# Optimization experiments

Measured on AMD Instinct MI355X. Metric: run time of the kernel, lower is better.

Reference implementation:

```python
import jax, jax.numpy as jnp
import numpy as np

BS, N, N_HEAD, F_IN, F_OUT = 8, 1024, 8, 256, 64
NEG_SLOPE = 0.2


def setup_inputs() -> dict:
    key = jax.random.key(0)
    k_h, k_adj, k_w, k_src, k_dst = jax.random.split(key, 5)
    h = jax.random.normal(k_h, (BS, N, F_IN), dtype=jnp.float32)
    adj = jax.random.randint(k_adj, (BS, N, N), 0, 2) > 0  # bool adjacency
    # xavier_uniform-style params
    def xavier(k, shape, fan_in, fan_out):
        limit = float(np.sqrt(6.0 / (fan_in + fan_out)))
        return jax.random.uniform(k, shape, jnp.float32, -limit, limit)
    w = xavier(k_w, (N_HEAD, F_IN, F_OUT), F_IN, F_OUT)
    a_src = xavier(k_src, (N_HEAD, F_OUT, 1), F_OUT, 1)
    a_dst = xavier(k_dst, (N_HEAD, F_OUT, 1), F_OUT, 1)
    bias = jnp.zeros((F_OUT,), dtype=jnp.float32)
    return {"h": h, "adj": adj, "w": w, "a_src": a_src, "a_dst": a_dst, "bias": bias}


def reference(h, adj, w, a_src, a_dst, bias):
    # h: [bs, n, f_in], w: [n_head, f_in, f_out]
    h_prime = jnp.einsum('bnf,hfo->bhno', h, w)            # [bs, h, n, f_out]
    t = jnp.tanh(h_prime)
    attn_src = jnp.einsum('bhno,ho->bhn', t, a_src[..., 0])  # [bs, h, n]
    attn_dst = jnp.einsum('bhno,ho->bhn', t, a_dst[..., 0])  # [bs, h, n]
    attn = attn_src[:, :, :, None] + attn_dst[:, :, None, :]  # [bs, h, n, n]
    attn = jnp.where(attn >= 0, attn, NEG_SLOPE * attn)       # leaky_relu(0.2)
    n = adj.shape[-1]
    mask = ~(adj[:, None, :, :] | jnp.eye(n, dtype=bool))     # [bs, 1->h, n, n]
    attn = jnp.where(mask, -jnp.inf, attn)
    attn = jax.nn.softmax(attn, axis=-1)                      # diag always valid
    out = jnp.einsum('bhnm,bhmo->bhno', attn, h_prime)
    return out + bias
```

## Files before the change

### kernel.cpp

```cpp
#include <hip/hip_runtime.h>
#include <math.h>

#define BS 8
#define NPTS 1024
#define NH 8
#define FIN 256
#define FOUT 64

typedef __attribute__((ext_vector_type(8))) short s8v;
typedef __attribute__((ext_vector_type(8))) _Float16 h8v;
typedef __attribute__((ext_vector_type(2))) __fp16 fp16x2;
typedef __attribute__((ext_vector_type(4))) float f4v;
typedef unsigned long long u64;

__device__ __forceinline__ unsigned short f2bf(float f) {
  unsigned u = __float_as_uint(f);
  return (unsigned short)((u + 0x7fffu + ((u >> 16) & 1u)) >> 16);
}
__device__ __forceinline__ float bf2f(unsigned short s) {
  return __uint_as_float(((unsigned)s) << 16);
}
__device__ __forceinline__ float fast_tanh(float x) {
  float e = __expf(2.f * x);
  return 1.f - 2.f / (e + 1.f);
}
__device__ __forceinline__ float hw_exp2(float x) {
  float r;
  asm("v_exp_f32 %0, %1" : "=v"(r) : "v"(x));
  return r;
}

__device__ __forceinline__ void gl_lds16(const void* g, void* l) {
  __builtin_amdgcn_global_load_lds(
      (const __attribute__((address_space(1))) unsigned*)g,
      (__attribute__((address_space(3))) unsigned*)l, 16, 0, 0);
}

__global__ __launch_bounds__(256) void prep_kernel(
    const void* __restrict__ adjv, const float* __restrict__ w,
    const float* __restrict__ h,
    u64* __restrict__ abits,
    unsigned short* __restrict__ wT_hi, unsigned short* __restrict__ wT_lo,
    unsigned short* __restrict__ hs_hi, unsigned short* __restrict__ hs_lo)
{
  const int blk = blockIdx.x;
  const int t = threadIdx.x;
  if (blk < 2048) {
    __shared__ int badsh;
    if (t == 0) badsh = 0;
    __syncthreads();
    if (((const unsigned*)adjv)[t] > 1u) badsh = 1;
    __syncthreads();
    const int lane = t & 63;
    const int gw = blk * 4 + (t >> 6);
    const int b = gw >> 10, i = gw & 1023;
    const int m16 = lane & 15, g = lane >> 4;
    u64 words[4];
    if (badsh == 0) {
      const int4* row4 = (const int4*)((const int*)adjv + ((size_t)b * NPTS + i) * NPTS);
      int4 av[4];
      av[0] = row4[lane]; av[1] = row4[lane + 64];
      av[2] = row4[lane + 128]; av[3] = row4[lane + 192];
#pragma unroll
      for (int ci = 0; ci < 4; ++ci) {
        unsigned n = (unsigned)(av[ci].x != 0) | ((unsigned)(av[ci].y != 0) << 1) |
                     ((unsigned)(av[ci].z != 0) << 2) | ((unsigned)(av[ci].w != 0) << 3);
        unsigned d = (unsigned)(i - (ci * 256 + 4 * lane));
        if (d < 4u) n |= 1u << d;
        u64 val = (u64)n << (4 * m16);
#pragma unroll
        for (int msk = 1; msk <= 8; msk <<= 1)
          val |= (u64)__shfl_xor(val, msk, 64);
        words[ci] = val;
      }
    } else {
      const unsigned* rowB = (const unsigned*)((const unsigned char*)adjv + ((size_t)b * NPTS + i) * NPTS);
      unsigned av[4];
      av[0] = rowB[lane]; av[1] = rowB[lane + 64];
      av[2] = rowB[lane + 128]; av[3] = rowB[lane + 192];
#pragma unroll
      for (int ci = 0; ci < 4; ++ci) {
        unsigned v = av[ci];
        unsigned n = ((v & 0xffu) ? 1u : 0u) | (((v >> 8) & 0xffu) ? 2u : 0u) |
                     (((v >> 16) & 0xffu) ? 4u : 0u) | ((v >> 24) ? 8u : 0u);
        unsigned d = (unsigned)(i - (ci * 256 + 4 * lane));
        if (d < 4u) n |= 1u << d;
        u64 val = (u64)n << (4 * m16);
#pragma unroll
        for (int msk = 1; msk <= 8; msk <<= 1)
          val |= (u64)__shfl_xor(val, msk, 64);
        words[ci] = val;
      }
    }
    if (m16 == 0) {
#pragma unroll
      for (int ci = 0; ci < 4; ++ci)
        abits[((size_t)b * NPTS + i) * 16 + ci * 4 + g] = words[ci];
    }
  } else if (blk < 2112) {
    const int bb = blk - 2048;
    const int hh = bb >> 3, ks = bb & 7;
    const int o = t & 63, kq = t >> 6;
#pragma unroll
    for (int e = 0; e < 8; ++e) {
      int k = ks * 32 + kq * 8 + e;
      float v = w[((size_t)hh * FIN + k) * FOUT + o];
      unsigned short hi = f2bf(v);
      wT_hi[((size_t)hh * FOUT + o) * FIN + k] = hi;
      wT_lo[((size_t)hh * FOUT + o) * FIN + k] = f2bf(v - bf2f(hi));
    }
  } else {
    const size_t g = (size_t)(blk - 2112) * 256 + t;
    const float4* hp4 = (const float4*)h + g * 2;
    float4 v0 = hp4[0], v1 = hp4[1];
    float vv[8] = {v0.x, v0.y, v0.z, v0.w, v1.x, v1.y, v1.z, v1.w};
    unsigned short hb[8], lb[8];
#pragma unroll
    for (int e = 0; e < 8; ++e) {
      unsigned u = __float_as_uint(vv[e]);
      float r = vv[e] - __uint_as_float(u & 0xffff0000u);
      hb[e] = (unsigned short)(u >> 16);
      lb[e] = (unsigned short)(__float_as_uint(r) >> 16);
    }
    *(uint4*)(hs_hi + g * 8) = *(const uint4*)&hb[0];
    *(uint4*)(hs_lo + g * 8) = *(const uint4*)&lb[0];
  }
}

__global__ __launch_bounds__(256, 4) void proj_kernel(
    const unsigned short* __restrict__ hs_hi, const unsigned short* __restrict__ hs_lo,
    const unsigned short* __restrict__ wT_hi, const unsigned short* __restrict__ wT_lo,
    const float* __restrict__ a_src, const float* __restrict__ a_dst,
    unsigned short* __restrict__ hfrag,
    float* __restrict__ srcb, float* __restrict__ dstb)
{
  __shared__ unsigned short Bbuf[2][4096];
  __shared__ float tile[64][65];

  const int t = threadIdx.x;
  const int lane = t & 63;
  const int wv = t >> 6;
  const int blk = blockIdx.x;
  const int it = blk & 15;
  const int hh = (blk >> 4) & 7;
  const int b  = blk >> 7;
  const int i0 = it * 64;
  const int bh = b * NH + hh;
  const int l15 = lane & 15;
  const int g4  = lane >> 4;
  const int koff = g4 * 8;

  const int o_t  = t >> 2;
  const int gsrc = (t & 3) ^ ((o_t >> 1) & 3);
  const unsigned short* gB_hi = wT_hi + ((size_t)(hh * FOUT + o_t)) * FIN + gsrc * 8;
  const unsigned short* gB_lo = wT_lo + ((size_t)(hh * FOUT + o_t)) * FIN + gsrc * 8;

  const unsigned short* arow_hi = hs_hi + ((size_t)(b * NPTS + i0 + wv * 16 + l15)) * FIN + koff;
  const unsigned short* arow_lo = hs_lo + ((size_t)(b * NPTS + i0 + wv * 16 + l15)) * FIN + koff;

  const int sw = (l15 >> 1) & 3;
  int roff[4];
#pragma unroll
  for (int nt = 0; nt < 4; ++nt)
    roff[nt] = (nt * 16 + l15) * 32 + (g4 ^ sw) * 8;

  gl_lds16(gB_hi, &Bbuf[0][wv * 512]);
  gl_lds16(gB_lo, &Bbuf[0][2048 + wv * 512]);
  s8v Ah = *(const s8v*)(arow_hi);
  s8v Al = *(const s8v*)(arow_lo);

  f4v acc[4];
#pragma unroll
  for (int nt = 0; nt < 4; ++nt) acc[nt] = 0.0f;
  __syncthreads();

#pragma unroll
  for (int k0 = 0; k0 < 8; ++k0) {
    const int buf = k0 & 1;
    s8v Ah_n = Ah, Al_n = Al;
    if (k0 < 7) {
      gl_lds16(gB_hi + (k0 + 1) * 32, &Bbuf[buf ^ 1][wv * 512]);
      gl_lds16(gB_lo + (k0 + 1) * 32, &Bbuf[buf ^ 1][2048 + wv * 512]);
      Ah_n = *(const s8v*)(arow_hi + (k0 + 1) * 32);
      Al_n = *(const s8v*)(arow_lo + (k0 + 1) * 32);
    }
    const unsigned short* fb = &Bbuf[buf][0];
#pragma unroll
    for (int nt = 0; nt < 4; ++nt) {
      s8v Bh = *(const s8v*)(fb + roff[nt]);
      s8v Bl = *(const s8v*)(fb + 2048 + roff[nt]);
      acc[nt] = __builtin_amdgcn_mfma_f32_16x16x32_bf16(Ah, Bh, acc[nt], 0, 0, 0);
      acc[nt] = __builtin_amdgcn_mfma_f32_16x16x32_bf16(Al, Bh, acc[nt], 0, 0, 0);
      acc[nt] = __builtin_amdgcn_mfma_f32_16x16x32_bf16(Ah, Bl, acc[nt], 0, 0, 0);
    }
    Ah = Ah_n; Al = Al_n;
    __syncthreads();
  }

  float a_s[4], a_d[4];
#pragma unroll
  for (int nt = 0; nt < 4; ++nt) {
    a_s[nt] = a_src[hh * FOUT + nt * 16 + l15];
    a_d[nt] = a_dst[hh * FOUT + nt * 16 + l15];
  }
#pragma unroll
  for (int qq = 0; qq < 4; ++qq) {
    float ps = 0.f, pd = 0.f;
#pragma unroll
    for (int nt = 0; nt < 4; ++nt) {
      float tv = fast_tanh(acc[nt][qq]);
      ps = fmaf(tv, a_s[nt], ps);
      pd = fmaf(tv, a_d[nt], pd);
    }
#pragma unroll
    for (int m = 8; m >= 1; m >>= 1) {
      ps += __shfl_xor(ps, m, 64);
      pd += __shfl_xor(pd, m, 64);
    }
    if (l15 == 0) {
      int row = i0 + wv * 16 + g4 * 4 + qq;
      srcb[(size_t)bh * NPTS + row] = ps;
      dstb[(size_t)bh * NPTS + row] = pd;
    }
  }

#pragma unroll
  for (int nt = 0; nt < 4; ++nt)
#pragma unroll
    for (int qq = 0; qq < 4; ++qq)
      tile[wv * 16 + g4 * 4 + qq][nt * 16 + l15] = acc[nt][qq];
  __syncthreads();

  const int cbase = t >> 6;
#pragma unroll
  for (int ci = 0; ci < 2; ++ci) {
    int cc = cbase + ci * 4;
    int ks = cc >> 2, nt2 = cc & 3;
    int jb = ks * 32 + ((lane >> 4) * 8);
    int ob = nt2 * 16 + l15;
    h8v v;
#pragma unroll
    for (int e = 0; e < 8; ++e) v[e] = (_Float16)tile[jb + e][ob];
    *(h8v*)(hfrag + (((size_t)(bh * 16 + it) * 8 + cc) * 64 + lane) * 8) = v;
  }
}

__global__ __launch_bounds__(256, 4) void attn_kernel(
    const u64* __restrict__ abits,
    const unsigned short* __restrict__ hfrag,
    const float* __restrict__ srcb, const float* __restrict__ dstb,
    const float* __restrict__ bias, float* __restrict__ out)
{
  __shared__ float dsh[NPTS];
  __shared__ float wred[4];
  __shared__ uint2 mlut[16];
  __shared__ unsigned short frag[2][4096];

  const int t = threadIdx.x;
  const int lane = t & 63;
  const int wv = t >> 6;
  const int blk = blockIdx.x;
  const int it = blk & 15;
  const int hh = (blk >> 4) & 7;
  const int b  = blk >> 7;
  const int i0 = it * 64;
  const int bh = b * NH + hh;
  const int l15 = lane & 15;
  const int koff = (lane >> 4) * 8;
  const int rowA = i0 + wv * 16 + l15;

  const uint4* fgb = (const uint4*)hfrag + (size_t)bh * 16 * 512;
  const u64* abrow = abits + ((size_t)b * NPTS + rowA) * 16;

  uint4 s0 = fgb[t];
  uint4 s1 = fgb[t + 256];
  u64 ab_cur = abrow[0];
  const float src_r = srcb[(size_t)bh * NPTS + rowA];
  float4 dv = ((const float4*)(dstb + (size_t)bh * NPTS))[t];

  if (t < 16) {
    unsigned m = t;
    mlut[t] = make_uint2(
        ((m & 1u) ? 0xFFFFu : 0u) | (((m >> 1) & 1u) ? 0xFFFF0000u : 0u),
        (((m >> 2) & 1u) ? 0xFFFFu : 0u) | (((m >> 3) & 1u) ? 0xFFFF0000u : 0u));
  }

  const float L2E = 1.44269504f;
  float4 dsc;
  dsc.x = dv.x * L2E; dsc.y = dv.y * L2E; dsc.z = dv.z * L2E; dsc.w = dv.w * L2E;
  ((float4*)dsh)[t] = dsc;
  float lm = fmaxf(fmaxf(dv.x, dv.y), fmaxf(dv.z, dv.w));
#pragma unroll
  for (int m = 32; m >= 1; m >>= 1) lm = fmaxf(lm, __shfl_xor(lm, m, 64));
  if (lane == 0) wred[wv] = lm;
  __syncthreads();
  const float M = fmaxf(fmaxf(wred[0], wred[1]), fmaxf(wred[2], wred[3]));
  const float xm = src_r + M;
  const float m_row = fmaxf(xm, 0.2f * xm);
  const float c1s = (src_r - m_row) * L2E;
  const float c2s = (0.2f * src_r - m_row) * L2E;

  ((uint4*)&frag[0][0])[t]       = s0;
  ((uint4*)&frag[0][0])[t + 256] = s1;
  __syncthreads();

  h8v ones;
#pragma unroll
  for (int e = 0; e < 8; ++e) ones[e] = (_Float16)1.0f;

  f4v acc[4], acc_l;
#pragma unroll
  for (int nt = 0; nt < 4; ++nt) acc[nt] = 0.0f;
  acc_l = 0.0f;

#pragma unroll 2
  for (int jt = 0; jt < 16; ++jt) {
    const int buf = jt & 1;
    uint4 n0, n1; u64 ab_nxt;
    if (jt < 15) {
      const uint4* fgn = fgb + (size_t)(jt + 1) * 512;
      n0 = fgn[t];
      n1 = fgn[t + 256];
      ab_nxt = abrow[jt + 1];
    }
    __builtin_amdgcn_sched_barrier(0);

    const int jb = jt * 64 + koff;
    float4 d0 = *(const float4*)&dsh[jb];
    float4 d1 = *(const float4*)&dsh[jb + 4];
    float4 d2 = *(const float4*)&dsh[jb + 32];
    float4 d3 = *(const float4*)&dsh[jb + 36];
    float dl0[8] = {d0.x, d0.y, d0.z, d0.w, d1.x, d1.y, d1.z, d1.w};
    float dl1[8] = {d2.x, d2.y, d2.z, d2.w, d3.x, d3.y, d3.z, d3.w};
    const unsigned w0 = (unsigned)(ab_cur) >> koff;
    const unsigned w1 = (unsigned)(ab_cur >> 32) >> koff;
    float pe0[8], pe1[8];
#pragma unroll
    for (int e = 0; e < 8; ++e) {
      float arg = fmaxf(c1s + dl0[e], fmaf(0.2f, dl0[e], c2s));
      pe0[e] = hw_exp2(arg);
    }
#pragma unroll
    for (int e = 0; e < 8; ++e) {
      float arg = fmaxf(c1s + dl1[e], fmaf(0.2f, dl1[e], c2s));
      pe1[e] = hw_exp2(arg);
    }
    union { fp16x2 q[4]; unsigned u[4]; h8v v; } ua, ub;
    ua.q[0] = __builtin_amdgcn_cvt_pkrtz(pe0[0], pe0[1]);
    ua.q[1] = __builtin_amdgcn_cvt_pkrtz(pe0[2], pe0[3]);
    ua.q[2] = __builtin_amdgcn_cvt_pkrtz(pe0[4], pe0[5]);
    ua.q[3] = __builtin_amdgcn_cvt_pkrtz(pe0[6], pe0[7]);
    ub.q[0] = __builtin_amdgcn_cvt_pkrtz(pe1[0], pe1[1]);
    ub.q[1] = __builtin_amdgcn_cvt_pkrtz(pe1[2], pe1[3]);
    ub.q[2] = __builtin_amdgcn_cvt_pkrtz(pe1[4], pe1[5]);
    ub.q[3] = __builtin_amdgcn_cvt_pkrtz(pe1[6], pe1[7]);
    {
      uint2 ma0 = mlut[w0 & 15], ma1 = mlut[(w0 >> 4) & 15];
      uint2 mb0 = mlut[w1 & 15], mb1 = mlut[(w1 >> 4) & 15];
      ua.u[0] &= ma0.x; ua.u[1] &= ma0.y; ua.u[2] &= ma1.x; ua.u[3] &= ma1.y;
      ub.u[0] &= mb0.x; ub.u[1] &= mb0.y; ub.u[2] &= mb1.x; ub.u[3] &= mb1.y;
    }
    h8v pa0 = ua.v;
    h8v pa1 = ub.v;

    __builtin_amdgcn_s_setprio(1);
#pragma unroll
    for (int nt = 0; nt < 4; ++nt) {
      h8v B0 = *(const h8v*)&frag[buf][(nt * 64 + lane) * 8];
      acc[nt] = __builtin_amdgcn_mfma_f32_16x16x32_f16(pa0, B0, acc[nt], 0, 0, 0);
    }
    acc_l = __builtin_amdgcn_mfma_f32_16x16x32_f16(pa0, ones, acc_l, 0, 0, 0);
#pragma unroll
    for (int nt = 0; nt < 4; ++nt) {
      h8v B1 = *(const h8v*)&frag[buf][((4 + nt) * 64 + lane) * 8];
      acc[nt] = __builtin_amdgcn_mfma_f32_16x16x32_f16(pa1, B1, acc[nt], 0, 0, 0);
    }
    acc_l = __builtin_amdgcn_mfma_f32_16x16x32_f16(pa1, ones, acc_l, 0, 0, 0);
    __builtin_amdgcn_s_setprio(0);

    if (jt < 15) {
      ((uint4*)&frag[buf ^ 1][0])[t]       = n0;
      ((uint4*)&frag[buf ^ 1][0])[t + 256] = n1;
      ab_cur = ab_nxt;
    }
    __syncthreads();
  }

  float bias4[4];
#pragma unroll
  for (int nt = 0; nt < 4; ++nt) bias4[nt] = bias[nt * 16 + l15];

#pragma unroll
  for (int qq = 0; qq < 4; ++qq) {
    float linv = 1.0f / acc_l[qq];
    int rowq = i0 + wv * 16 + (lane >> 4) * 4 + qq;
    size_t ob = ((size_t)bh * NPTS + rowq) * FOUT;
#pragma unroll
    for (int nt = 0; nt < 4; ++nt)
      out[ob + nt * 16 + l15] = acc[nt][qq] * linv + bias4[nt];
  }
}

extern "C" void kernel_launch(void* const* d_in, const int* in_sizes, int n_in,
                              void* d_out, int out_size, void* d_ws, size_t ws_size,
                              hipStream_t stream)
{
  const float* h     = (const float*)d_in[0];
  const void*  adj   = d_in[1];
  const float* w     = (const float*)d_in[2];
  const float* a_src = (const float*)d_in[3];
  const float* a_dst = (const float*)d_in[4];
  const float* bias  = (const float*)d_in[5];
  float* out = (float*)d_out;

  char* p = (char*)d_ws;
  float* srcb = (float*)p;                      p += (size_t)BS * NH * NPTS * 4;
  float* dstb = (float*)p;                      p += (size_t)BS * NH * NPTS * 4;
  unsigned short* wT_hi = (unsigned short*)p;   p += (size_t)NH * FOUT * FIN * 2;
  unsigned short* wT_lo = (unsigned short*)p;   p += (size_t)NH * FOUT * FIN * 2;
  u64* abits = (u64*)p;                         p += (size_t)BS * NPTS * 16 * 8;
  unsigned short* hs_hi = (unsigned short*)p;   p += (size_t)BS * NPTS * FIN * 2;
  unsigned short* hs_lo = (unsigned short*)p;   p += (size_t)BS * NPTS * FIN * 2;
  unsigned short* hfrag = (unsigned short*)p;

  prep_kernel<<<dim3(3136), dim3(256), 0, stream>>>(
      adj, w, h, abits, wT_hi, wT_lo, hs_hi, hs_lo);
  proj_kernel<<<dim3(1024), dim3(256), 0, stream>>>(
      hs_hi, hs_lo, wT_hi, wT_lo, a_src, a_dst, hfrag, srcb, dstb);
  attn_kernel<<<dim3(1024), dim3(256), 0, stream>>>(
      abits, hfrag, srcb, dstb, bias, out);
}
```

Before: 52.07 us.

## Factor softmax exponentials into per-row and per-column terms; triple-buffer projection loads

```diff
diff --git a/kernel.cpp b/kernel.cpp
--- a/kernel.cpp
+++ b/kernel.cpp
@@ -127,6 +127,11 @@
   }
 }
 
+union ProjSmem {
+  unsigned short Bbuf[3][4096];
+  float tile[64][65];
+};
+
 __global__ __launch_bounds__(256, 4) void proj_kernel(
     const unsigned short* __restrict__ hs_hi, const unsigned short* __restrict__ hs_lo,
     const unsigned short* __restrict__ wT_hi, const unsigned short* __restrict__ wT_lo,
@@ -134,8 +139,7 @@
     unsigned short* __restrict__ hfrag,
     float* __restrict__ srcb, float* __restrict__ dstb)
 {
-  __shared__ unsigned short Bbuf[2][4096];
-  __shared__ float tile[64][65];
+  __shared__ ProjSmem sm;
 
   const int t = threadIdx.x;
   const int lane = t & 63;
@@ -164,38 +168,48 @@
   for (int nt = 0; nt < 4; ++nt)
     roff[nt] = (nt * 16 + l15) * 32 + (g4 ^ sw) * 8;
 
-  gl_lds16(gB_hi, &Bbuf[0][wv * 512]);
-  gl_lds16(gB_lo, &Bbuf[0][2048 + wv * 512]);
-  s8v Ah = *(const s8v*)(arow_hi);
-  s8v Al = *(const s8v*)(arow_lo);
+  s8v Ah[3], Al[3];
+  gl_lds16(gB_hi, &sm.Bbuf[0][wv * 512]);
+  gl_lds16(gB_lo, &sm.Bbuf[0][2048 + wv * 512]);
+  Ah[0] = *(const s8v*)(arow_hi);
+  Al[0] = *(const s8v*)(arow_lo);
+  gl_lds16(gB_hi + 32, &sm.Bbuf[1][wv * 512]);
+  gl_lds16(gB_lo + 32, &sm.Bbuf[1][2048 + wv * 512]);
+  Ah[1] = *(const s8v*)(arow_hi + 32);
+  Al[1] = *(const s8v*)(arow_lo + 32);
 
   f4v acc[4];
 #pragma unroll
   for (int nt = 0; nt < 4; ++nt) acc[nt] = 0.0f;
-  __syncthreads();
 
 #pragma unroll
   for (int k0 = 0; k0 < 8; ++k0) {
-    const int buf = k0 & 1;
-    s8v Ah_n = Ah, Al_n = Al;
-    if (k0 < 7) {
-      gl_lds16(gB_hi + (k0 + 1) * 32, &Bbuf[buf ^ 1][wv * 512]);
-      gl_lds16(gB_lo + (k0 + 1) * 32, &Bbuf[buf ^ 1][2048 + wv * 512]);
-      Ah_n = *(const s8v*)(arow_hi + (k0 + 1) * 32);
-      Al_n = *(const s8v*)(arow_lo + (k0 + 1) * 32);
-    }
-    const unsigned short* fb = &Bbuf[buf][0];
+    if (k0 == 7) asm volatile("s_waitcnt vmcnt(0)" ::: "memory");
+    else         asm volatile("s_waitcnt vmcnt(4)" ::: "memory");
+    __builtin_amdgcn_sched_barrier(0);
+    __builtin_amdgcn_s_barrier();
+    __builtin_amdgcn_sched_barrier(0);
+
+    if (k0 < 6) {
+      const int nb = (k0 + 2) % 3;
+      gl_lds16(gB_hi + (k0 + 2) * 32, &sm.Bbuf[nb][wv * 512]);
+      gl_lds16(gB_lo + (k0 + 2) * 32, &sm.Bbuf[nb][2048 + wv * 512]);
+      Ah[nb] = *(const s8v*)(arow_hi + (k0 + 2) * 32);
+      Al[nb] = *(const s8v*)(arow_lo + (k0 + 2) * 32);
+    }
+
+    const int cb = k0 % 3;
+    const unsigned short* fb = &sm.Bbuf[cb][0];
 #pragma unroll
     for (int nt = 0; nt < 4; ++nt) {
       s8v Bh = *(const s8v*)(fb + roff[nt]);
       s8v Bl = *(const s8v*)(fb + 2048 + roff[nt]);
-      acc[nt] = __builtin_amdgcn_mfma_f32_16x16x32_bf16(Ah, Bh, acc[nt], 0, 0, 0);
-      acc[nt] = __builtin_amdgcn_mfma_f32_16x16x32_bf16(Al, Bh, acc[nt], 0, 0, 0);
-      acc[nt] = __builtin_amdgcn_mfma_f32_16x16x32_bf16(Ah, Bl, acc[nt], 0, 0, 0);
-    }
-    Ah = Ah_n; Al = Al_n;
-    __syncthreads();
-  }
+      acc[nt] = __builtin_amdgcn_mfma_f32_16x16x32_bf16(Ah[cb], Bh, acc[nt], 0, 0, 0);
+      acc[nt] = __builtin_amdgcn_mfma_f32_16x16x32_bf16(Al[cb], Bh, acc[nt], 0, 0, 0);
+      acc[nt] = __builtin_amdgcn_mfma_f32_16x16x32_bf16(Ah[cb], Bl, acc[nt], 0, 0, 0);
+    }
+  }
+  __syncthreads();
 
   float a_s[4], a_d[4];
 #pragma unroll
@@ -228,7 +242,7 @@
   for (int nt = 0; nt < 4; ++nt)
 #pragma unroll
     for (int qq = 0; qq < 4; ++qq)
-      tile[wv * 16 + g4 * 4 + qq][nt * 16 + l15] = acc[nt][qq];
+      sm.tile[wv * 16 + g4 * 4 + qq][nt * 16 + l15] = acc[nt][qq];
   __syncthreads();
 
   const int cbase = t >> 6;
@@ -240,7 +254,7 @@
     int ob = nt2 * 16 + l15;
     h8v v;
 #pragma unroll
-    for (int e = 0; e < 8; ++e) v[e] = (_Float16)tile[jb + e][ob];
+    for (int e = 0; e < 8; ++e) v[e] = (_Float16)sm.tile[jb + e][ob];
     *(h8v*)(hfrag + (((size_t)(bh * 16 + it) * 8 + cc) * 64 + lane) * 8) = v;
   }
 }
@@ -251,7 +265,8 @@
     const float* __restrict__ srcb, const float* __restrict__ dstb,
     const float* __restrict__ bias, float* __restrict__ out)
 {
-  __shared__ float dsh[NPTS];
+  __shared__ float e1sh[NPTS];
+  __shared__ float e2sh[NPTS];
   __shared__ float wred[4];
   __shared__ uint2 mlut[16];
   __shared__ unsigned short frag[2][4096];
@@ -286,9 +301,15 @@
   }
 
   const float L2E = 1.44269504f;
-  float4 dsc;
-  dsc.x = dv.x * L2E; dsc.y = dv.y * L2E; dsc.z = dv.z * L2E; dsc.w = dv.w * L2E;
-  ((float4*)dsh)[t] = dsc;
+  {
+    float4 e1, e2;
+    e1.x = hw_exp2(dv.x * L2E);          e1.y = hw_exp2(dv.y * L2E);
+    e1.z = hw_exp2(dv.z * L2E);          e1.w = hw_exp2(dv.w * L2E);
+    e2.x = hw_exp2(dv.x * (0.2f * L2E)); e2.y = hw_exp2(dv.y * (0.2f * L2E));
+    e2.z = hw_exp2(dv.z * (0.2f * L2E)); e2.w = hw_exp2(dv.w * (0.2f * L2E));
+    ((float4*)e1sh)[t] = e1;
+    ((float4*)e2sh)[t] = e2;
+  }
   float lm = fmaxf(fmaxf(dv.x, dv.y), fmaxf(dv.z, dv.w));
 #pragma unroll
   for (int m = 32; m >= 1; m >>= 1) lm = fmaxf(lm, __shfl_xor(lm, m, 64));
@@ -297,8 +318,8 @@
   const float M = fmaxf(fmaxf(wred[0], wred[1]), fmaxf(wred[2], wred[3]));
   const float xm = src_r + M;
   const float m_row = fmaxf(xm, 0.2f * xm);
-  const float c1s = (src_r - m_row) * L2E;
-  const float c2s = (0.2f * src_r - m_row) * L2E;
+  const float Ai = hw_exp2((src_r - m_row) * L2E);
+  const float Bi = hw_exp2((0.2f * src_r - m_row) * L2E);
 
   ((uint4*)&frag[0][0])[t]       = s0;
   ((uint4*)&frag[0][0])[t + 256] = s1;
@@ -326,34 +347,35 @@
     __builtin_amdgcn_sched_barrier(0);
 
     const int jb = jt * 64 + koff;
-    float4 d0 = *(const float4*)&dsh[jb];
-    float4 d1 = *(const float4*)&dsh[jb + 4];
-    float4 d2 = *(const float4*)&dsh[jb + 32];
-    float4 d3 = *(const float4*)&dsh[jb + 36];
-    float dl0[8] = {d0.x, d0.y, d0.z, d0.w, d1.x, d1.y, d1.z, d1.w};
-    float dl1[8] = {d2.x, d2.y, d2.z, d2.w, d3.x, d3.y, d3.z, d3.w};
+    float4 ea0 = *(const float4*)&e1sh[jb];
+    float4 ea1 = *(const float4*)&e1sh[jb + 4];
+    float4 eb0 = *(const float4*)&e2sh[jb];
+    float4 eb1 = *(const float4*)&e2sh[jb + 4];
+    float4 ec0 = *(const float4*)&e1sh[jb + 32];
+    float4 ec1 = *(const float4*)&e1sh[jb + 36];
+    float4 ed0 = *(const float4*)&e2sh[jb + 32];
+    float4 ed1 = *(const float4*)&e2sh[jb + 36];
+    float p0[8] = {
+      fmaxf(Ai * ea0.x, Bi * eb0.x), fmaxf(Ai * ea0.y, Bi * eb0.y),
+      fmaxf(Ai * ea0.z, Bi * eb0.z), fmaxf(Ai * ea0.w, Bi * eb0.w),
+      fmaxf(Ai * ea1.x, Bi * eb1.x), fmaxf(Ai * ea1.y, Bi * eb1.y),
+      fmaxf(Ai * ea1.z, Bi * eb1.z), fmaxf(Ai * ea1.w, Bi * eb1.w)};
+    float p1[8] = {
+      fmaxf(Ai * ec0.x, Bi * ed0.x), fmaxf(Ai * ec0.y, Bi * ed0.y),
+      fmaxf(Ai * ec0.z, Bi * ed0.z), fmaxf(Ai * ec0.w, Bi * ed0.w),
+      fmaxf(Ai * ec1.x, Bi * ed1.x), fmaxf(Ai * ec1.y, Bi * ed1.y),
+      fmaxf(Ai * ec1.z, Bi * ed1.z), fmaxf(Ai * ec1.w, Bi * ed1.w)};
     const unsigned w0 = (unsigned)(ab_cur) >> koff;
     const unsigned w1 = (unsigned)(ab_cur >> 32) >> koff;
-    float pe0[8], pe1[8];
-#pragma unroll
-    for (int e = 0; e < 8; ++e) {
-      float arg = fmaxf(c1s + dl0[e], fmaf(0.2f, dl0[e], c2s));
-      pe0[e] = hw_exp2(arg);
-    }
-#pragma unroll
-    for (int e = 0; e < 8; ++e) {
-      float arg = fmaxf(c1s + dl1[e], fmaf(0.2f, dl1[e], c2s));
-      pe1[e] = hw_exp2(arg);
-    }
     union { fp16x2 q[4]; unsigned u[4]; h8v v; } ua, ub;
-    ua.q[0] = __builtin_amdgcn_cvt_pkrtz(pe0[0], pe0[1]);
-    ua.q[1] = __builtin_amdgcn_cvt_pkrtz(pe0[2], pe0[3]);
-    ua.q[2] = __builtin_amdgcn_cvt_pkrtz(pe0[4], pe0[5]);
-    ua.q[3] = __builtin_amdgcn_cvt_pkrtz(pe0[6], pe0[7]);
-    ub.q[0] = __builtin_amdgcn_cvt_pkrtz(pe1[0], pe1[1]);
-    ub.q[1] = __builtin_amdgcn_cvt_pkrtz(pe1[2], pe1[3]);
-    ub.q[2] = __builtin_amdgcn_cvt_pkrtz(pe1[4], pe1[5]);
-    ub.q[3] = __builtin_amdgcn_cvt_pkrtz(pe1[6], pe1[7]);
+    ua.q[0] = __builtin_amdgcn_cvt_pkrtz(p0[0], p0[1]);
+    ua.q[1] = __builtin_amdgcn_cvt_pkrtz(p0[2], p0[3]);
+    ua.q[2] = __builtin_amdgcn_cvt_pkrtz(p0[4], p0[5]);
+    ua.q[3] = __builtin_amdgcn_cvt_pkrtz(p0[6], p0[7]);
+    ub.q[0] = __builtin_amdgcn_cvt_pkrtz(p1[0], p1[1]);
+    ub.q[1] = __builtin_amdgcn_cvt_pkrtz(p1[2], p1[3]);
+    ub.q[2] = __builtin_amdgcn_cvt_pkrtz(p1[4], p1[5]);
+    ub.q[3] = __builtin_amdgcn_cvt_pkrtz(p1[6], p1[7]);
     {
       uint2 ma0 = mlut[w0 & 15], ma1 = mlut[(w0 >> 4) & 15];
       uint2 mb0 = mlut[w1 & 15], mb1 = mlut[(w1 >> 4) & 15];
```

After: 50.11 us. -3.8%, faster.
